# Kernel optimization log

Measured on AMD Instinct MI355X. Metric: run time of the kernel, lower is better.

The kernel has to match this reference:

```python
import jax, jax.numpy as jnp
import numpy as np
from jax import lax

B, T, N, C, AD, HW, KS, KT = 32, 8, 196, 768, 192, 14, 3, 3
EPS = 1e-5

def _groupnorm1(x, gamma, beta, axes):
    # GroupNorm(1, C): normalize over channel+spatial dims per sample
    mu = jnp.mean(x, axis=axes, keepdims=True)
    var = jnp.mean((x - mu) ** 2, axis=axes, keepdims=True)
    xn = (x - mu) * lax.rsqrt(var + EPS)
    shape = [1] * x.ndim
    shape[1] = -1
    return xn * gamma.reshape(shape) + beta.reshape(shape)

def setup_inputs() -> dict:
    key = jax.random.key(0)
    ks = jax.random.split(key, 16)
    s = 0.02
    return {
        'x': jax.random.normal(ks[0], (B, T, N + 1, C), jnp.float32),
        'w_down': jax.random.normal(ks[1], (C, AD), jnp.float32) * s,
        'b_down': jnp.zeros((AD,), jnp.float32),
        'w_sdw': jax.random.normal(ks[2], (AD, 1, KS, KS), jnp.float32) * s,
        'w_spw': jax.random.normal(ks[3], (AD, AD), jnp.float32) * s,  # [out,in]
        'g_snorm': jnp.ones((AD,), jnp.float32),
        'b_snorm': jnp.zeros((AD,), jnp.float32),
        'w_diff': jax.random.normal(ks[4], (AD, AD), jnp.float32) * s,  # [in,out]
        'w_tdw': jax.random.normal(ks[5], (AD, 1, KT), jnp.float32) * s,
        'w_tpw': jax.random.normal(ks[6], (AD, AD), jnp.float32) * s,  # [out,in]
        'g_tnorm': jnp.ones((AD,), jnp.float32),
        'b_tnorm': jnp.zeros((AD,), jnp.float32),
        'w_g1': jax.random.normal(ks[7], (AD, AD), jnp.float32) * s,
        'b_g1': jnp.zeros((AD,), jnp.float32),
        'w_g2': jax.random.normal(ks[8], (AD, AD), jnp.float32) * s,
        'b_g2': jnp.zeros((AD,), jnp.float32),
        'w_up': jax.random.normal(ks[9], (AD, C), jnp.float32) * s,  # torch zero-inits; randomized for nontrivial test
        'b_up': jnp.zeros((C,), jnp.float32),
        'w_cls': jax.random.normal(ks[10], (AD, C), jnp.float32) * s,
        'b_cls': jnp.zeros((C,), jnp.float32),
    }

def reference(x, w_down, b_down, w_sdw, w_spw, g_snorm, b_snorm, w_diff,
              w_tdw, w_tpw, g_tnorm, b_tnorm, w_g1, b_g1, w_g2, b_g2,
              w_up, b_up, w_cls, b_cls):
    gelu = lambda v: jax.nn.gelu(v, approximate=False)  # torch nn.GELU default (erf)
    cls_token = x[:, :, :1, :]
    patch = x[:, :, 1:, :]
    b, t, n, _ = patch.shape
    hw = HW
    ph = patch @ w_down + b_down  # [b,t,n,ad]
    ad = ph.shape[-1]
    # spatial path: (b t) c h w
    sp = ph.reshape(b * t, hw, hw, ad).transpose(0, 3, 1, 2)
    sp = lax.conv_general_dilated(sp, w_sdw, (1, 1), 'SAME',
                                  feature_group_count=ad,
                                  dimension_numbers=('NCHW', 'OIHW', 'NCHW'))
    sp = _groupnorm1(sp, g_snorm, b_snorm, axes=(1, 2, 3))
    sp = gelu(sp)
    sp = jnp.einsum('bchw,oc->bohw', sp, w_spw)
    spatial = sp.transpose(0, 2, 3, 1).reshape(b, t, n, ad)
    # diff gating
    diff = jnp.concatenate([jnp.zeros_like(ph[:, :1]), ph[:, 1:] - ph[:, :-1]], axis=1)
    diff = diff + diff @ w_diff
    # temporal path: (b n) c t
    tp = (ph + diff).transpose(0, 2, 3, 1).reshape(b * n, ad, t)
    tp = lax.conv_general_dilated(tp, w_tdw, (1,), 'SAME',
                                  feature_group_count=ad,
                                  dimension_numbers=('NCH', 'OIH', 'NCH'))
    tp = _groupnorm1(tp, g_tnorm, b_tnorm, axes=(1, 2))
    tp = gelu(tp)
    tp = jnp.einsum('bct,oc->bot', tp, w_tpw)
    temporal = tp.reshape(b, n, ad, t).transpose(0, 3, 1, 2)
    # gate
    gi = jnp.mean(jnp.abs(diff), axis=(1, 2))  # [b, ad]
    gate = jax.nn.sigmoid(gelu(gi @ w_g1 + b_g1) @ w_g2 + b_g2)[:, None, None, :]
    fused = gate * temporal + (1.0 - gate) * spatial
    patch_out = patch + fused @ w_up + b_up
    cls_ctx = jnp.mean(fused, axis=2, keepdims=True)
    cls_out = cls_token + cls_ctx @ w_cls + b_cls
    return jnp.concatenate([cls_out, patch_out], axis=2)
```

## Files before the change

### kernel.cpp

```cpp
#include <hip/hip_runtime.h>
#include <hip/hip_bf16.h>
#include <math.h>

typedef __attribute__((ext_vector_type(8))) short s8v;
typedef __attribute__((ext_vector_type(4))) short s4v;
typedef __attribute__((ext_vector_type(4))) float f4v;

#define GN_EPS 1e-5f

__device__ __forceinline__ float s2f(short s) {
    unsigned int u = ((unsigned int)(unsigned short)s) << 16;
    float f; __builtin_memcpy(&f, &u, 4); return f;
}
__device__ __forceinline__ short f2s(float f) {
    __hip_bfloat16 h = __float2bfloat16(f);
    short s; __builtin_memcpy(&s, &h, 2); return s;
}
__device__ __forceinline__ float gelu_f(float x) {
    return 0.5f * x * (1.0f + erff(x * 0.7071067811865476f));
}
__device__ __forceinline__ void gload16(const void* g, void* l) {
    __builtin_amdgcn_global_load_lds((const __attribute__((address_space(1))) void*)g,
                                     (__attribute__((address_space(3))) void*)l,
                                     16, 0, 0);
}

__global__ void detect_kernel(const unsigned int* g_snorm_raw, int* flag) {
    if (threadIdx.x == 0) flag[0] = (g_snorm_raw[0] == 0x3F800000u) ? 1 : 0;
}

struct ConvArgs {
    const void* src[19];
    int cum[20];
};
__global__ __launch_bounds__(256)
void convert_kernel(ConvArgs a, short* __restrict__ dst, const int* __restrict__ dflag,
                    int total) {
    const int dt = dflag[0];
    int idx = blockIdx.x * 256 + threadIdx.x;
    const int stride = gridDim.x * 256;
    for (; idx < total; idx += stride) {
        int seg = 0;
        while (idx >= a.cum[seg + 1]) seg++;
        const int off = idx - a.cum[seg];
        const float v = dt ? ((const float*)a.src[seg])[off]
                           : s2f(((const short*)a.src[seg])[off]);
        dst[idx] = f2s(v);
    }
}

__global__ __launch_bounds__(256)
void transpose_kernel(const short* __restrict__ src, short* __restrict__ dst,
                      int R, int C) {
    const int idx = blockIdx.x * 256 + threadIdx.x;
    if (idx < R * C) {
        const int r = idx / C, c = idx - r * C;
        dst[c * R + r] = src[idx];
    }
}


#define AMAP_PLAIN 0
#define AMAP_X     1
#define AMAP_DIFF  2
#define EPI_BIASH 0
#define EPI_H     1
#define EPI_DIFF  2
#define EPI_UP    3

template<int K_DIM, int N_DIM, int AMAP, int EPI>
__global__ __launch_bounds__(256)
void gemm_kernel(const void* __restrict__ Asrc, const short* __restrict__ Bmat,
                 const short* __restrict__ bias, const short* __restrict__ phH,
                 const void* __restrict__ xExt, short* __restrict__ outH,
                 void* __restrict__ outExt, float* __restrict__ giOut,
                 const int* __restrict__ dflag)
{
    const int dt = dflag[0];

    __shared__ short As[2][2048];
    __shared__ short Bs[2][2048];

    const int tid  = threadIdx.x;
    const int lane = tid & 63;
    const int wave = tid >> 6;
    const int wr = wave >> 1, wc = wave & 1;
    const int m16 = lane & 15, q = lane >> 4;
    const int rowBase = blockIdx.x * 64;
    const int colBase = blockIdx.y * 64;

    const int sr = tid >> 2;
    const int ss = tid & 3;
    const int sg = ss ^ ((sr >> 1) & 3);
    const int wOff = wave * 512;

    const int agrow = rowBase + sr;
    long aBase;
    int abt7 = 0;
    if constexpr (AMAP == AMAP_X) {
        const int bt = agrow / 196;
        aBase = (long)(agrow + bt + 1) * 768 + sg * 8;
    } else if constexpr (AMAP == AMAP_DIFF) {
        aBase = (long)agrow * K_DIM + sg * 8;
        abt7 = (agrow / 196) & 7;
    } else {
        aBase = (long)agrow * K_DIM + sg * 8;
    }
    const long bBase = (long)(colBase + sr) * K_DIM + sg * 8;

    const int ra = wr * 32 + m16;
    const int rb = wc * 32 + m16;
    const int oA0 = ra * 32 + (q ^ ((ra >> 1) & 3)) * 8;
    const int oB0 = rb * 32 + (q ^ ((rb >> 1) & 3)) * 8;
    const int oA1 = oA0 + 512;
    const int oB1 = oB0 + 512;

    f4v acc[2][2] = {};
    constexpr int NK = K_DIM / 32;

    auto stage = [&](int kk, int buf) {
        if constexpr (AMAP == AMAP_PLAIN) {
            gload16((const short*)Asrc + aBase + kk, (void*)&As[buf][wOff]);
        } else if constexpr (AMAP == AMAP_X) {
            if (dt) {
                const float* xp = (const float*)Asrc + aBase + kk;
                const float4 f0 = *(const float4*)xp;
                const float4 f1 = *(const float4*)(xp + 4);
                s8v av;
                av[0] = f2s(f0.x); av[1] = f2s(f0.y); av[2] = f2s(f0.z); av[3] = f2s(f0.w);
                av[4] = f2s(f1.x); av[5] = f2s(f1.y); av[6] = f2s(f1.z); av[7] = f2s(f1.w);
                *(s8v*)&As[buf][sr * 32 + ss * 8] = av;
            } else {
                gload16((const short*)Asrc + aBase + kk, (void*)&As[buf][wOff]);
            }
        } else {
            s8v av;
            if (abt7) {
                const short* p1 = (const short*)Asrc + aBase + kk;
                const s8v v1 = *(const s8v*)p1;
                const s8v v0 = *(const s8v*)(p1 - 37632);
                #pragma unroll
                for (int j = 0; j < 8; j++) av[j] = f2s(s2f(v1[j]) - s2f(v0[j]));
            } else {
                #pragma unroll
                for (int j = 0; j < 8; j++) av[j] = 0;
            }
            *(s8v*)&As[buf][sr * 32 + ss * 8] = av;
        }
        gload16(Bmat + bBase + kk, (void*)&Bs[buf][wOff]);
    };

    stage(0, 0);
    __syncthreads();

    int cur = 0;
    for (int t = 0; t < NK; ++t) {
        if (t + 1 < NK) stage((t + 1) * 32, cur ^ 1);

        const s8v afr0 = *(const s8v*)&As[cur][oA0];
        const s8v afr1 = *(const s8v*)&As[cur][oA1];
        const s8v bfr0 = *(const s8v*)&Bs[cur][oB0];
        const s8v bfr1 = *(const s8v*)&Bs[cur][oB1];

        acc[0][0] = __builtin_amdgcn_mfma_f32_16x16x32_bf16(bfr0, afr0, acc[0][0], 0, 0, 0);
        acc[0][1] = __builtin_amdgcn_mfma_f32_16x16x32_bf16(bfr1, afr0, acc[0][1], 0, 0, 0);
        acc[1][0] = __builtin_amdgcn_mfma_f32_16x16x32_bf16(bfr0, afr1, acc[1][0], 0, 0, 0);
        acc[1][1] = __builtin_amdgcn_mfma_f32_16x16x32_bf16(bfr1, afr1, acc[1][1], 0, 0, 0);

        __syncthreads();
        cur ^= 1;
    }

    #pragma unroll
    for (int i = 0; i < 2; i++) {
        const int grow = rowBase + wr * 32 + i * 16 + m16;
        const int gcb  = colBase + wc * 32 + q * 4;

        if constexpr (EPI == EPI_BIASH) {
            #pragma unroll
            for (int j = 0; j < 2; j++) {
                const int gc = gcb + j * 16;
                const s4v bv = *(const s4v*)&bias[gc];
                s4v o;
                #pragma unroll
                for (int r = 0; r < 4; r++) o[r] = f2s(acc[i][j][r] + s2f(bv[r]));
                *(s4v*)&outH[(long)grow * N_DIM + gc] = o;
            }
        } else if constexpr (EPI == EPI_H) {
            #pragma unroll
            for (int j = 0; j < 2; j++) {
                const int gc = gcb + j * 16;
                s4v o;
                #pragma unroll
                for (int r = 0; r < 4; r++) o[r] = f2s(acc[i][j][r]);
                *(s4v*)&outH[(long)grow * N_DIM + gc] = o;
            }
        } else if constexpr (EPI == EPI_DIFF) {
            const int t = (grow / 196) & 7;
            float ga[8];
            #pragma unroll
            for (int j = 0; j < 2; j++) {
                const int gc = gcb + j * 16;
                const long pOff = (long)grow * 192 + gc;
                const s4v p1 = *(const s4v*)&phH[pOff];
                s4v p0 = p1;
                if (t > 0) p0 = *(const s4v*)&phH[pOff - 37632];
                s4v o;
                #pragma unroll
                for (int r = 0; r < 4; r++) {
                    const float phv = s2f(p1[r]);
                    const float d = (t > 0) ? (phv - s2f(p0[r])) : 0.0f;
                    const float tpmp = acc[i][j][r] + d;
                    ga[j * 4 + r] = fabsf(tpmp);
                    o[r] = f2s(tpmp + phv);
                }
                *(s4v*)&outH[pOff] = o;
            }
            #pragma unroll
            for (int mlt = 1; mlt < 16; mlt <<= 1) {
                #pragma unroll
                for (int k = 0; k < 8; k++) ga[k] += __shfl_xor(ga[k], mlt, 64);
            }
            if (m16 == 0) {
                const int b = (rowBase + wr * 32 + i * 16) / 1568;
                #pragma unroll
                for (int k = 0; k < 8; k++) {
                    const int col = colBase + wc * 32 + (k >> 2) * 16 + q * 4 + (k & 3);
                    atomicAdd(&giOut[b * 192 + col], ga[k]);
                }
            }
        } else {
            const int bt = grow / 196;
            const long orow = (long)(grow + bt + 1) * 768;
            #pragma unroll
            for (int j = 0; j < 2; j++) {
                const int gc = gcb + j * 16;
                const s4v bv = *(const s4v*)&bias[gc];
                if (dt) {
                    const float4 xv = *(const float4*)((const float*)xExt + orow + gc);
                    float4 ov;
                    ov.x = xv.x + acc[i][j][0] + s2f(bv[0]);
                    ov.y = xv.y + acc[i][j][1] + s2f(bv[1]);
                    ov.z = xv.z + acc[i][j][2] + s2f(bv[2]);
                    ov.w = xv.w + acc[i][j][3] + s2f(bv[3]);
                    *(float4*)((float*)outExt + orow + gc) = ov;
                } else {
                    const s4v xv = *(const s4v*)((const short*)xExt + orow + gc);
                    s4v ov;
                    #pragma unroll
                    for (int r = 0; r < 4; r++)
                        ov[r] = f2s(s2f(xv[r]) + acc[i][j][r] + s2f(bv[r]));
                    *(s4v*)((short*)outExt + orow + gc) = ov;
                }
            }
        }
    }
}

__global__ __launch_bounds__(1024, 4)
void spatial_kernel(const short* __restrict__ ph, const short* __restrict__ w_sdw,
                    const short* __restrict__ g_s, const short* __restrict__ b_s,
                    short* __restrict__ snorm)
{
    __shared__ short tile[196 * 192];
    __shared__ short wkT[9 * 192];
    __shared__ float gsl[192], bsl[192];
    __shared__ float redA[16], redB[16];
    __shared__ float stats[2];

    const int bt = blockIdx.x, tid = threadIdx.x;
    const short* Pg = ph + (long)bt * 37632;

    for (int i = tid; i < 4704; i += 1024)
        *(s8v*)&tile[i * 8] = *(const s8v*)&Pg[i * 8];
    for (int i = tid; i < 1728; i += 1024) {
        const int c = i / 9, tap = i - c * 9;
        wkT[tap * 192 + c] = w_sdw[i];
    }
    if (tid < 192) { gsl[tid] = s2f(g_s[tid]); bsl[tid] = s2f(b_s[tid]); }
    __syncthreads();

    float val[5][8];
    float lsum = 0.f, lsq = 0.f;
    #pragma unroll
    for (int it = 0; it < 5; it++) {
        const int i = tid + it * 1024;
        #pragma unroll
        for (int k = 0; k < 8; k++) val[it][k] = 0.f;
        if (i < 4704) {
            const int n = i / 24, c8 = i - n * 24;
            const int h = n / 14, w = n - (n / 14) * 14;
            float a[8] = {0.f,0.f,0.f,0.f,0.f,0.f,0.f,0.f};
            #pragma unroll
            for (int tap = 0; tap < 9; tap++) {
                const int dh = tap / 3 - 1, dw = tap % 3 - 1;
                const int hh = h + dh, ww = w + dw;
                if (hh >= 0 && hh < 14 && ww >= 0 && ww < 14) {
                    s8v iv = *(const s8v*)&tile[(hh * 14 + ww) * 192 + c8 * 8];
                    s8v wv = *(const s8v*)&wkT[tap * 192 + c8 * 8];
                    #pragma unroll
                    for (int k = 0; k < 8; k++) a[k] += s2f(iv[k]) * s2f(wv[k]);
                }
            }
            #pragma unroll
            for (int k = 0; k < 8; k++) {
                val[it][k] = a[k]; lsum += a[k]; lsq += a[k] * a[k];
            }
        }
    }
    #pragma unroll
    for (int d = 1; d < 64; d <<= 1) {
        lsum += __shfl_xor(lsum, d, 64);
        lsq  += __shfl_xor(lsq,  d, 64);
    }
    if ((tid & 63) == 0) { redA[tid >> 6] = lsum; redB[tid >> 6] = lsq; }
    __syncthreads();
    if (tid < 64) {
        float s = (tid < 16) ? redA[tid] : 0.f;
        float qq = (tid < 16) ? redB[tid] : 0.f;
        #pragma unroll
        for (int d = 1; d < 16; d <<= 1) {
            s  += __shfl_xor(s,  d, 64);
            qq += __shfl_xor(qq, d, 64);
        }
        if (tid == 0) {
            const float inv = 1.0f / 37632.0f;
            const float mean = s * inv;
            const float var  = qq * inv - mean * mean;
            stats[0] = mean; stats[1] = rsqrtf(var + GN_EPS);
        }
    }
    __syncthreads();
    const float mean = stats[0], rstd = stats[1];
    short* Og = snorm + (long)bt * 37632;
    #pragma unroll
    for (int it = 0; it < 5; it++) {
        const int i = tid + it * 1024;
        if (i < 4704) {
            const int c8 = i - (i / 24) * 24;
            s8v o;
            #pragma unroll
            for (int k = 0; k < 8; k++) {
                const int c = c8 * 8 + k;
                const float y = (val[it][k] - mean) * rstd * gsl[c] + bsl[c];
                o[k] = f2s(gelu_f(y));
            }
            *(s8v*)&Og[i * 8] = o;
        }
    }
}

__global__ __launch_bounds__(192)
void temporal_kernel(const short* __restrict__ tp, const short* __restrict__ w_tdw,
                     const short* __restrict__ g_t, const short* __restrict__ b_t,
                     short* __restrict__ tnorm)
{
    const int bn = blockIdx.x;
    const int c = threadIdx.x;
    const int b = bn / 196, n = bn - (bn / 196) * 196;
    const long base = ((long)b * 8 * 196 + n) * 192 + c;
    const long ts = 196 * 192;
    float v[8], o[8];
    #pragma unroll
    for (int t = 0; t < 8; t++) v[t] = s2f(tp[base + t * ts]);
    const float w0 = s2f(w_tdw[c * 3]), w1 = s2f(w_tdw[c * 3 + 1]), w2 = s2f(w_tdw[c * 3 + 2]);
    #pragma unroll
    for (int t = 0; t < 8; t++) {
        float a = v[t] * w1;
        if (t > 0) a += v[t - 1] * w0;
        if (t < 7) a += v[t + 1] * w2;
        o[t] = a;
    }
    float lsum = 0.f, lsq = 0.f;
    #pragma unroll
    for (int t = 0; t < 8; t++) { lsum += o[t]; lsq += o[t] * o[t]; }
    __shared__ float red1[192], red2[192];
    red1[c] = lsum; red2[c] = lsq;
    __syncthreads();
    for (int s = 96; s > 2; s >>= 1) {
        if (c < s) { red1[c] += red1[c + s]; red2[c] += red2[c + s]; }
        __syncthreads();
    }
    const float mean = (red1[0] + red1[1] + red1[2]) * (1.0f / 1536.0f);
    const float var  = (red2[0] + red2[1] + red2[2]) * (1.0f / 1536.0f) - mean * mean;
    const float rstd = rsqrtf(var + GN_EPS);
    const float gg = s2f(g_t[c]), bb = s2f(b_t[c]);
    #pragma unroll
    for (int t = 0; t < 8; t++) {
        const float y = (o[t] - mean) * rstd * gg + bb;
        tnorm[base + t * ts] = f2s(gelu_f(y));
    }
}

__global__ __launch_bounds__(192)
void gate_kernel(const float* __restrict__ gi, const short* __restrict__ w_g1,
                 const short* __restrict__ b_g1, const short* __restrict__ w_g2,
                 const short* __restrict__ b_g2, float* __restrict__ gate)
{
    const int b = blockIdx.x, o = threadIdx.x;
    __shared__ float s0[192], s1[192];
    s0[o] = gi[b * 192 + o] * (1.0f / 1568.0f);
    __syncthreads();
    float a = s2f(b_g1[o]);
    for (int cc = 0; cc < 192; cc++) a += s0[cc] * s2f(w_g1[cc * 192 + o]);
    s1[o] = gelu_f(a);
    __syncthreads();
    float a2 = s2f(b_g2[o]);
    for (int cc = 0; cc < 192; cc++) a2 += s1[cc] * s2f(w_g2[cc * 192 + o]);
    gate[b * 192 + o] = 1.0f / (1.0f + expf(-a2));
}

__global__ __launch_bounds__(192)
void fuse_kernel(const short* __restrict__ temporal, const short* __restrict__ spatial,
                 const float* __restrict__ gate, short* __restrict__ fused,
                 float* __restrict__ cls_sum)
{
    const int bt = blockIdx.x;
    const int b = bt >> 3;
    const int tid = threadIdx.x;
    const int c8 = tid >> 3, sub = tid & 7;
    float g[8];
    {
        const float4* gp = (const float4*)&gate[b * 192 + c8 * 8];
        float4 ga = gp[0], gb = gp[1];
        g[0]=ga.x; g[1]=ga.y; g[2]=ga.z; g[3]=ga.w;
        g[4]=gb.x; g[5]=gb.y; g[6]=gb.z; g[7]=gb.w;
    }
    float part[8] = {0.f,0.f,0.f,0.f,0.f,0.f,0.f,0.f};
    for (int n = sub; n < 196; n += 8) {
        const long off = ((long)bt * 196 + n) * 192 + c8 * 8;
        s8v tv = *(const s8v*)(temporal + off);
        s8v sv = *(const s8v*)(spatial + off);
        s8v fv;
        #pragma unroll
        for (int k = 0; k < 8; k++) {
            const float f = g[k] * s2f(tv[k]) + (1.0f - g[k]) * s2f(sv[k]);
            fv[k] = f2s(f);
            part[k] += f;
        }
        *(s8v*)(fused + off) = fv;
    }
    #pragma unroll
    for (int d = 1; d < 8; d <<= 1) {
        #pragma unroll
        for (int k = 0; k < 8; k++) part[k] += __shfl_xor(part[k], d, 64);
    }
    if (sub == 0) {
        #pragma unroll
        for (int k = 0; k < 8; k++)
            cls_sum[bt * 192 + c8 * 8 + k] = part[k] * (1.0f / 196.0f);
    }
}

__global__ __launch_bounds__(256)
void cls_kernel(const float* __restrict__ cls_sum, const short* __restrict__ w_cls,
                const short* __restrict__ b_cls, const void* __restrict__ x,
                void* __restrict__ out, const int* __restrict__ dflag)
{
    const int dt = dflag[0];
    const int bt = blockIdx.x, tid = threadIdx.x;
    __shared__ float ctx[192];
    if (tid < 192) ctx[tid] = cls_sum[bt * 192 + tid];
    __syncthreads();
    for (int oc = tid; oc < 768; oc += 256) {
        float a = s2f(b_cls[oc]);
        for (int cc = 0; cc < 192; cc++) a += ctx[cc] * s2f(w_cls[cc * 768 + oc]);
        const long oi = (long)bt * 197 * 768 + oc;
        if (dt) ((float*)out)[oi] = ((const float*)x)[oi] + a;
        else    ((short*)out)[oi] = f2s(s2f(((const short*)x)[oi]) + a);
    }
}

extern "C" void kernel_launch(void* const* d_in, const int* in_sizes, int n_in,
                              void* d_out, int out_size, void* d_ws, size_t ws_size,
                              hipStream_t stream) {
    const void* x = d_in[0];

    const long F = 50176L * 192L;
    short* wsS = (short*)d_ws;
    short* P = wsS;
    short* Q = wsS + F;
    short* R = wsS + 2 * F;
    short* S = wsS + 3 * F;
    short* W = wsS + 4 * F;
    int cum[20]; cum[0] = 0;
    for (int i = 1; i <= 19; i++) cum[i] = cum[i - 1] + in_sizes[i];
    const int totalW = cum[19];

    short* WT   = W + ((totalW + 7) & ~7);
    short* wdT  = WT;
    short* wdfT = WT + 147456;
    short* wupT = WT + 147456 + 36864;

    float* smalls = (float*)(WT + 331776);
    float* gi      = smalls;
    float* gate    = smalls + 6144;
    float* cls_sum = smalls + 12288;
    int*   dflag   = (int*)(smalls + 61440);

    const short* b_down = W + cum[1];
    const short* w_sdw  = W + cum[2];
    const short* w_spw  = W + cum[3];
    const short* g_sn   = W + cum[4];
    const short* b_sn   = W + cum[5];
    const short* w_tdw  = W + cum[7];
    const short* w_tpw  = W + cum[8];
    const short* g_tn   = W + cum[9];
    const short* b_tn   = W + cum[10];
    const short* w_g1   = W + cum[11];
    const short* b_g1   = W + cum[12];
    const short* w_g2   = W + cum[13];
    const short* b_g2   = W + cum[14];
    const short* b_up   = W + cum[16];
    const short* w_cls  = W + cum[17];
    const short* b_cls  = W + cum[18];

    hipMemsetAsync(gi, 0, 6144 * sizeof(float), stream);
    detect_kernel<<<1, 64, 0, stream>>>((const unsigned int*)d_in[5], dflag);

    ConvArgs ca;
    for (int i = 0; i < 19; i++) ca.src[i] = d_in[i + 1];
    for (int i = 0; i < 20; i++) ca.cum[i] = cum[i];
    convert_kernel<<<618, 256, 0, stream>>>(ca, W, dflag, totalW);

    transpose_kernel<<<576, 256, 0, stream>>>(W + cum[0],  wdT,  768, 192);
    transpose_kernel<<<144, 256, 0, stream>>>(W + cum[6],  wdfT, 192, 192);
    transpose_kernel<<<576, 256, 0, stream>>>(W + cum[15], wupT, 192, 768);

    dim3 g3(784, 3), g12(784, 12);

    gemm_kernel<768, 192, AMAP_X, EPI_BIASH>
        <<<g3, 256, 0, stream>>>(x, wdT, b_down, nullptr, nullptr, P, nullptr, nullptr, dflag);
    spatial_kernel<<<256, 1024, 0, stream>>>(P, w_sdw, g_sn, b_sn, R);
    gemm_kernel<192, 192, AMAP_PLAIN, EPI_H>
        <<<g3, 256, 0, stream>>>(R, w_spw, nullptr, nullptr, nullptr, S, nullptr, nullptr, dflag);
    gemm_kernel<192, 192, AMAP_DIFF, EPI_DIFF>
        <<<g3, 256, 0, stream>>>(P, wdfT, nullptr, P, nullptr, Q, nullptr, gi, dflag);
    temporal_kernel<<<6272, 192, 0, stream>>>(Q, w_tdw, g_tn, b_tn, R);
    gemm_kernel<192, 192, AMAP_PLAIN, EPI_H>
        <<<g3, 256, 0, stream>>>(R, w_tpw, nullptr, nullptr, nullptr, Q, nullptr, nullptr, dflag);
    gate_kernel<<<32, 192, 0, stream>>>(gi, w_g1, b_g1, w_g2, b_g2, gate);
    fuse_kernel<<<256, 192, 0, stream>>>(Q, S, gate, R, cls_sum);
    gemm_kernel<192, 768, AMAP_PLAIN, EPI_UP>
        <<<g12, 256, 0, stream>>>(R, wupT, b_up, nullptr, x, nullptr, d_out, nullptr, dflag);
    cls_kernel<<<256, 256, 0, stream>>>(cls_sum, w_cls, b_cls, x, d_out, dflag);
}
```

Baseline: 620.5 us.

## Retile GEMMs to full-width blocks with triple-buffered async LDS pipeline

The GEMM kernel is templated on block tile size. The 192-wide GEMMs now use 64x192 tiles so each A tile is loaded only once, and the up-projection uses 128x128 tiles. The main loop becomes a 3-stage LDS pipeline with explicit vmcnt waits and raw barriers instead of a double buffer with __syncthreads. The fp32 A and diff paths prefetch one step ahead in registers, and the x read and output write in the epilogue use nontemporal loads and stores. Together these aim to cut redundant A reads and hide global-load latency, at the cost of more registers and LDS per block, which may lower occupancy.

```diff
diff --git a/kernel.cpp b/kernel.cpp
--- a/kernel.cpp
+++ b/kernel.cpp
@@ -24,6 +24,15 @@
                                      (__attribute__((address_space(3))) void*)l,
                                      16, 0, 0);
 }
+template<int N> __device__ __forceinline__ void wait_vm() {
+    if constexpr (N == 0) asm volatile("s_waitcnt vmcnt(0)" ::: "memory");
+    else if constexpr (N == 4) asm volatile("s_waitcnt vmcnt(4)" ::: "memory");
+    else if constexpr (N == 5) asm volatile("s_waitcnt vmcnt(5)" ::: "memory");
+    else if constexpr (N == 6) asm volatile("s_waitcnt vmcnt(6)" ::: "memory");
+    else asm volatile("s_waitcnt vmcnt(0)" ::: "memory");
+}
+__device__ __forceinline__ void wait_lgkm0() { asm volatile("s_waitcnt lgkmcnt(0)" ::: "memory"); }
+__device__ __forceinline__ void bar() { __builtin_amdgcn_s_barrier(); }
 
 __global__ void detect_kernel(const unsigned int* g_snorm_raw, int* flag) {
     if (threadIdx.x == 0) flag[0] = (g_snorm_raw[0] == 0x3F800000u) ? 1 : 0;
@@ -68,139 +77,234 @@
 #define EPI_DIFF  2
 #define EPI_UP    3
 
-template<int K_DIM, int N_DIM, int AMAP, int EPI>
-__global__ __launch_bounds__(256)
+template<int BM, int BN, int K_DIM, int N_DIM, int AMAP, int EPI>
+__global__ __launch_bounds__(256, 3)
 void gemm_kernel(const void* __restrict__ Asrc, const short* __restrict__ Bmat,
                  const short* __restrict__ bias, const short* __restrict__ phH,
                  const void* __restrict__ xExt, short* __restrict__ outH,
                  void* __restrict__ outExt, float* __restrict__ giOut,
                  const int* __restrict__ dflag)
 {
+    constexpr int WR = BM / 2, WC = BN / 2;
+    constexpr int FM = WR / 16, FN = WC / 16;
+    constexpr int AL = BM / 64;
+    constexpr int BL = BN / 64;
+    constexpr int NK = K_DIM / 32;
+    constexpr int ASZ = BM * 32, BSZ = BN * 32;
+    constexpr int GL = AL + BL;
+    constexpr int RL = 2 * AL + BL;
+
     const int dt = dflag[0];
 
-    __shared__ short As[2][2048];
-    __shared__ short Bs[2][2048];
+    __shared__ short As[3 * ASZ];
+    __shared__ short Bs[3 * BSZ];
 
     const int tid  = threadIdx.x;
     const int lane = tid & 63;
     const int wave = tid >> 6;
     const int wr = wave >> 1, wc = wave & 1;
     const int m16 = lane & 15, q = lane >> 4;
-    const int rowBase = blockIdx.x * 64;
-    const int colBase = blockIdx.y * 64;
+    const int rowBase = blockIdx.x * BM;
+    const int colBase = blockIdx.y * BN;
 
     const int sr = tid >> 2;
     const int ss = tid & 3;
     const int sg = ss ^ ((sr >> 1) & 3);
     const int wOff = wave * 512;
 
-    const int agrow = rowBase + sr;
-    long aBase;
-    int abt7 = 0;
-    if constexpr (AMAP == AMAP_X) {
-        const int bt = agrow / 196;
-        aBase = (long)(agrow + bt + 1) * 768 + sg * 8;
-    } else if constexpr (AMAP == AMAP_DIFF) {
-        aBase = (long)agrow * K_DIM + sg * 8;
-        abt7 = (agrow / 196) & 7;
+    long aBase[AL]; int abt7[AL];
+    #pragma unroll
+    for (int l = 0; l < AL; l++) {
+        const int grow = rowBase + sr + 64 * l;
+        if constexpr (AMAP == AMAP_X) {
+            const int bt = grow / 196;
+            aBase[l] = (long)(grow + bt + 1) * 768 + sg * 8;
+            abt7[l] = 0;
+        } else if constexpr (AMAP == AMAP_DIFF) {
+            aBase[l] = (long)grow * K_DIM + sg * 8;
+            abt7[l] = (grow / 196) & 7;
+        } else {
+            aBase[l] = (long)grow * K_DIM + sg * 8;
+            abt7[l] = 0;
+        }
+    }
+    long bBase[BL];
+    #pragma unroll
+    for (int l = 0; l < BL; l++)
+        bBase[l] = (long)(colBase + sr + 64 * l) * K_DIM + sg * 8;
+
+    const int ra0 = wr * WR + m16;
+    const int rb0 = wc * WC + m16;
+    const int oA0 = ra0 * 32 + (q ^ ((ra0 >> 1) & 3)) * 8;
+    const int oB0 = rb0 * 32 + (q ^ ((rb0 >> 1) & 3)) * 8;
+
+    f4v acc[FM][FN] = {};
+
+    auto compute = [&](int aOff, int bOff) {
+        s8v af[FM], bf[FN];
+        #pragma unroll
+        for (int i = 0; i < FM; i++) af[i] = *(const s8v*)&As[aOff + oA0 + i * 512];
+        #pragma unroll
+        for (int j = 0; j < FN; j++) bf[j] = *(const s8v*)&Bs[bOff + oB0 + j * 512];
+        #pragma unroll
+        for (int i = 0; i < FM; i++)
+            #pragma unroll
+            for (int j = 0; j < FN; j++)
+                acc[i][j] = __builtin_amdgcn_mfma_f32_16x16x32_bf16(bf[j], af[i], acc[i][j], 0, 0, 0);
+    };
+    auto gstageB = [&](int kk, int buf) {
+        #pragma unroll
+        for (int l = 0; l < BL; l++)
+            gload16(Bmat + bBase[l] + kk, (void*)&Bs[buf * BSZ + l * 2048 + wOff]);
+    };
+    auto gstageA = [&](int kk, int buf) {
+        #pragma unroll
+        for (int l = 0; l < AL; l++)
+            gload16((const short*)Asrc + aBase[l] + kk, (void*)&As[buf * ASZ + l * 2048 + wOff]);
+    };
+
+    if constexpr (AMAP == AMAP_PLAIN) {
+        gstageA(0, 0);  gstageB(0, 0);
+        gstageA(32, 1); gstageB(32, 1);
+        wait_vm<GL>(); bar();
+        int bi = 0;
+        for (int t = 0; t < NK - 2; ++t) {
+            int b2 = bi + 2; if (b2 >= 3) b2 -= 3;
+            gstageA((t + 2) * 32, b2); gstageB((t + 2) * 32, b2);
+            compute(bi * ASZ, bi * BSZ);
+            wait_vm<GL>(); bar();
+            bi = (bi + 1 == 3) ? 0 : bi + 1;
+        }
+        compute(bi * ASZ, bi * BSZ);
+        wait_vm<0>(); bar();
+        bi = (bi + 1 == 3) ? 0 : bi + 1;
+        compute(bi * ASZ, bi * BSZ);
+    } else if constexpr (AMAP == AMAP_X) {
+        if (dt == 0) {
+            gstageA(0, 0);  gstageB(0, 0);
+            gstageA(32, 1); gstageB(32, 1);
+            wait_vm<GL>(); bar();
+            int bi = 0;
+            for (int t = 0; t < NK - 2; ++t) {
+                int b2 = bi + 2; if (b2 >= 3) b2 -= 3;
+                gstageA((t + 2) * 32, b2); gstageB((t + 2) * 32, b2);
+                compute(bi * ASZ, bi * BSZ);
+                wait_vm<GL>(); bar();
+                bi = (bi + 1 == 3) ? 0 : bi + 1;
+            }
+            compute(bi * ASZ, bi * BSZ);
+            wait_vm<0>(); bar();
+            bi = (bi + 1 == 3) ? 0 : bi + 1;
+            compute(bi * ASZ, bi * BSZ);
+        } else {
+            f4v ra0v, ra1v, rb0v, rb1v;
+            auto loadA = [&](int kk, f4v& r0, f4v& r1) {
+                const float* xp = (const float*)Asrc + aBase[0] + kk;
+                r0 = __builtin_nontemporal_load((const f4v*)xp);
+                r1 = __builtin_nontemporal_load((const f4v*)(xp + 4));
+            };
+            auto writeA = [&](int idx, const f4v& r0, const f4v& r1) {
+                s8v av;
+                av[0] = f2s(r0.x); av[1] = f2s(r0.y); av[2] = f2s(r0.z); av[3] = f2s(r0.w);
+                av[4] = f2s(r1.x); av[5] = f2s(r1.y); av[6] = f2s(r1.z); av[7] = f2s(r1.w);
+                *(s8v*)&As[idx * ASZ + tid * 8] = av;
+            };
+            loadA(0, ra0v, ra1v); gstageB(0, 0);
+            wait_vm<0>();
+            writeA(0, ra0v, ra1v);
+            loadA(32, ra0v, ra1v); gstageB(32, 1);
+            wait_lgkm0(); bar();
+            int bi = 0;
+            for (int t = 0; t < NK - 2; ++t) {
+                int b2 = bi + 2; if (b2 >= 3) b2 -= 3;
+                loadA((t + 2) * 32, rb0v, rb1v); gstageB((t + 2) * 32, b2);
+                compute((t & 1) * ASZ, bi * BSZ);
+                wait_vm<RL>();
+                writeA((t + 1) & 1, ra0v, ra1v);
+                wait_lgkm0(); bar();
+                ra0v = rb0v; ra1v = rb1v;
+                bi = (bi + 1 == 3) ? 0 : bi + 1;
+            }
+            compute(((NK - 2) & 1) * ASZ, bi * BSZ);
+            wait_vm<0>();
+            writeA((NK - 1) & 1, ra0v, ra1v);
+            wait_lgkm0(); bar();
+            bi = (bi + 1 == 3) ? 0 : bi + 1;
+            compute(((NK - 1) & 1) * ASZ, bi * BSZ);
+        }
     } else {
-        aBase = (long)agrow * K_DIM + sg * 8;
-    }
-    const long bBase = (long)(colBase + sr) * K_DIM + sg * 8;
-
-    const int ra = wr * 32 + m16;
-    const int rb = wc * 32 + m16;
-    const int oA0 = ra * 32 + (q ^ ((ra >> 1) & 3)) * 8;
-    const int oB0 = rb * 32 + (q ^ ((rb >> 1) & 3)) * 8;
-    const int oA1 = oA0 + 512;
-    const int oB1 = oB0 + 512;
-
-    f4v acc[2][2] = {};
-    constexpr int NK = K_DIM / 32;
-
-    auto stage = [&](int kk, int buf) {
-        if constexpr (AMAP == AMAP_PLAIN) {
-            gload16((const short*)Asrc + aBase + kk, (void*)&As[buf][wOff]);
-        } else if constexpr (AMAP == AMAP_X) {
-            if (dt) {
-                const float* xp = (const float*)Asrc + aBase + kk;
-                const float4 f0 = *(const float4*)xp;
-                const float4 f1 = *(const float4*)(xp + 4);
-                s8v av;
-                av[0] = f2s(f0.x); av[1] = f2s(f0.y); av[2] = f2s(f0.z); av[3] = f2s(f0.w);
-                av[4] = f2s(f1.x); av[5] = f2s(f1.y); av[6] = f2s(f1.z); av[7] = f2s(f1.w);
-                *(s8v*)&As[buf][sr * 32 + ss * 8] = av;
-            } else {
-                gload16((const short*)Asrc + aBase + kk, (void*)&As[buf][wOff]);
-            }
-        } else {
+        s8v ra1v, ra0v, rb1v, rb0v;
+        auto loadA = [&](int kk, s8v& v1, s8v& v0) {
+            const short* p1 = (const short*)Asrc + aBase[0] + kk;
+            const short* p0 = p1 - (abt7[0] ? 37632 : 0);
+            v1 = *(const s8v*)p1;
+            v0 = *(const s8v*)p0;
+        };
+        auto writeA = [&](int idx, const s8v& v1, const s8v& v0) {
             s8v av;
-            if (abt7) {
-                const short* p1 = (const short*)Asrc + aBase + kk;
-                const s8v v1 = *(const s8v*)p1;
-                const s8v v0 = *(const s8v*)(p1 - 37632);
+            if (abt7[0]) {
                 #pragma unroll
                 for (int j = 0; j < 8; j++) av[j] = f2s(s2f(v1[j]) - s2f(v0[j]));
             } else {
                 #pragma unroll
                 for (int j = 0; j < 8; j++) av[j] = 0;
             }
-            *(s8v*)&As[buf][sr * 32 + ss * 8] = av;
-        }
-        gload16(Bmat + bBase + kk, (void*)&Bs[buf][wOff]);
-    };
-
-    stage(0, 0);
-    __syncthreads();
-
-    int cur = 0;
-    for (int t = 0; t < NK; ++t) {
-        if (t + 1 < NK) stage((t + 1) * 32, cur ^ 1);
-
-        const s8v afr0 = *(const s8v*)&As[cur][oA0];
-        const s8v afr1 = *(const s8v*)&As[cur][oA1];
-        const s8v bfr0 = *(const s8v*)&Bs[cur][oB0];
-        const s8v bfr1 = *(const s8v*)&Bs[cur][oB1];
-
-        acc[0][0] = __builtin_amdgcn_mfma_f32_16x16x32_bf16(bfr0, afr0, acc[0][0], 0, 0, 0);
-        acc[0][1] = __builtin_amdgcn_mfma_f32_16x16x32_bf16(bfr1, afr0, acc[0][1], 0, 0, 0);
-        acc[1][0] = __builtin_amdgcn_mfma_f32_16x16x32_bf16(bfr0, afr1, acc[1][0], 0, 0, 0);
-        acc[1][1] = __builtin_amdgcn_mfma_f32_16x16x32_bf16(bfr1, afr1, acc[1][1], 0, 0, 0);
-
-        __syncthreads();
-        cur ^= 1;
-    }
-
-    #pragma unroll
-    for (int i = 0; i < 2; i++) {
-        const int grow = rowBase + wr * 32 + i * 16 + m16;
-        const int gcb  = colBase + wc * 32 + q * 4;
+            *(s8v*)&As[idx * ASZ + tid * 8] = av;
+        };
+        loadA(0, ra1v, ra0v); gstageB(0, 0);
+        wait_vm<0>();
+        writeA(0, ra1v, ra0v);
+        loadA(32, ra1v, ra0v); gstageB(32, 1);
+        wait_lgkm0(); bar();
+        int bi = 0;
+        for (int t = 0; t < NK - 2; ++t) {
+            int b2 = bi + 2; if (b2 >= 3) b2 -= 3;
+            loadA((t + 2) * 32, rb1v, rb0v); gstageB((t + 2) * 32, b2);
+            compute((t & 1) * ASZ, bi * BSZ);
+            wait_vm<RL>();
+            writeA((t + 1) & 1, ra1v, ra0v);
+            wait_lgkm0(); bar();
+            ra1v = rb1v; ra0v = rb0v;
+            bi = (bi + 1 == 3) ? 0 : bi + 1;
+        }
+        compute(((NK - 2) & 1) * ASZ, bi * BSZ);
+        wait_vm<0>();
+        writeA((NK - 1) & 1, ra1v, ra0v);
+        wait_lgkm0(); bar();
+        bi = (bi + 1 == 3) ? 0 : bi + 1;
+        compute(((NK - 1) & 1) * ASZ, bi * BSZ);
+    }
+
+    #pragma unroll
+    for (int fi = 0; fi < FM; fi++) {
+        const int grow = rowBase + wr * WR + fi * 16 + m16;
+        const int gcb  = colBase + wc * WC + q * 4;
 
         if constexpr (EPI == EPI_BIASH) {
             #pragma unroll
-            for (int j = 0; j < 2; j++) {
-                const int gc = gcb + j * 16;
+            for (int fj = 0; fj < FN; fj++) {
+                const int gc = gcb + fj * 16;
                 const s4v bv = *(const s4v*)&bias[gc];
                 s4v o;
                 #pragma unroll
-                for (int r = 0; r < 4; r++) o[r] = f2s(acc[i][j][r] + s2f(bv[r]));
+                for (int r = 0; r < 4; r++) o[r] = f2s(acc[fi][fj][r] + s2f(bv[r]));
                 *(s4v*)&outH[(long)grow * N_DIM + gc] = o;
             }
         } else if constexpr (EPI == EPI_H) {
             #pragma unroll
-            for (int j = 0; j < 2; j++) {
-                const int gc = gcb + j * 16;
+            for (int fj = 0; fj < FN; fj++) {
+                const int gc = gcb + fj * 16;
                 s4v o;
                 #pragma unroll
-                for (int r = 0; r < 4; r++) o[r] = f2s(acc[i][j][r]);
+                for (int r = 0; r < 4; r++) o[r] = f2s(acc[fi][fj][r]);
                 *(s4v*)&outH[(long)grow * N_DIM + gc] = o;
             }
         } else if constexpr (EPI == EPI_DIFF) {
             const int t = (grow / 196) & 7;
-            float ga[8];
-            #pragma unroll
-            for (int j = 0; j < 2; j++) {
-                const int gc = gcb + j * 16;
+            float ga[FN * 4];
+            #pragma unroll
+            for (int fj = 0; fj < FN; fj++) {
+                const int gc = gcb + fj * 16;
                 const long pOff = (long)grow * 192 + gc;
                 const s4v p1 = *(const s4v*)&phH[pOff];
                 s4v p0 = p1;
@@ -210,8 +314,8 @@
                 for (int r = 0; r < 4; r++) {
                     const float phv = s2f(p1[r]);
                     const float d = (t > 0) ? (phv - s2f(p0[r])) : 0.0f;
-                    const float tpmp = acc[i][j][r] + d;
-                    ga[j * 4 + r] = fabsf(tpmp);
+                    const float tpmp = acc[fi][fj][r] + d;
+                    ga[fj * 4 + r] = fabsf(tpmp);
                     o[r] = f2s(tpmp + phv);
                 }
                 *(s4v*)&outH[pOff] = o;
@@ -219,13 +323,13 @@
             #pragma unroll
             for (int mlt = 1; mlt < 16; mlt <<= 1) {
                 #pragma unroll
-                for (int k = 0; k < 8; k++) ga[k] += __shfl_xor(ga[k], mlt, 64);
+                for (int k = 0; k < FN * 4; k++) ga[k] += __shfl_xor(ga[k], mlt, 64);
             }
             if (m16 == 0) {
-                const int b = (rowBase + wr * 32 + i * 16) / 1568;
+                const int b = (rowBase + wr * WR + fi * 16) / 1568;
                 #pragma unroll
-                for (int k = 0; k < 8; k++) {
-                    const int col = colBase + wc * 32 + (k >> 2) * 16 + q * 4 + (k & 3);
+                for (int k = 0; k < FN * 4; k++) {
+                    const int col = colBase + wc * WC + (k >> 2) * 16 + q * 4 + (k & 3);
                     atomicAdd(&giOut[b * 192 + col], ga[k]);
                 }
             }
@@ -233,23 +337,24 @@
             const int bt = grow / 196;
             const long orow = (long)(grow + bt + 1) * 768;
             #pragma unroll
-            for (int j = 0; j < 2; j++) {
-                const int gc = gcb + j * 16;
+            for (int fj = 0; fj < FN; fj++) {
+                const int gc = gcb + fj * 16;
                 const s4v bv = *(const s4v*)&bias[gc];
                 if (dt) {
-                    const float4 xv = *(const float4*)((const float*)xExt + orow + gc);
-                    float4 ov;
-                    ov.x = xv.x + acc[i][j][0] + s2f(bv[0]);
-                    ov.y = xv.y + acc[i][j][1] + s2f(bv[1]);
-                    ov.z = xv.z + acc[i][j][2] + s2f(bv[2]);
-                    ov.w = xv.w + acc[i][j][3] + s2f(bv[3]);
-                    *(float4*)((float*)outExt + orow + gc) = ov;
+                    const f4v xv = __builtin_nontemporal_load(
+                        (const f4v*)((const float*)xExt + orow + gc));
+                    f4v ov;
+                    ov.x = xv.x + acc[fi][fj][0] + s2f(bv[0]);
+                    ov.y = xv.y + acc[fi][fj][1] + s2f(bv[1]);
+                    ov.z = xv.z + acc[fi][fj][2] + s2f(bv[2]);
+                    ov.w = xv.w + acc[fi][fj][3] + s2f(bv[3]);
+                    __builtin_nontemporal_store(ov, (f4v*)((float*)outExt + orow + gc));
                 } else {
                     const s4v xv = *(const s4v*)((const short*)xExt + orow + gc);
                     s4v ov;
                     #pragma unroll
                     for (int r = 0; r < 4; r++)
-                        ov[r] = f2s(s2f(xv[r]) + acc[i][j][r] + s2f(bv[r]));
+                        ov[r] = f2s(s2f(xv[r]) + acc[fi][fj][r] + s2f(bv[r]));
                     *(s4v*)((short*)outExt + orow + gc) = ov;
                 }
             }
@@ -421,8 +526,8 @@
     const int c8 = tid >> 3, sub = tid & 7;
     float g[8];
     {
-        const float4* gp = (const float4*)&gate[b * 192 + c8 * 8];
-        float4 ga = gp[0], gb = gp[1];
+        const f4v* gp = (const f4v*)&gate[b * 192 + c8 * 8];
+        f4v ga = gp[0], gb = gp[1];
         g[0]=ga.x; g[1]=ga.y; g[2]=ga.z; g[3]=ga.w;
         g[4]=gb.x; g[5]=gb.y; g[6]=gb.z; g[7]=gb.w;
     }
@@ -527,21 +632,19 @@
     transpose_kernel<<<144, 256, 0, stream>>>(W + cum[6],  wdfT, 192, 192);
     transpose_kernel<<<576, 256, 0, stream>>>(W + cum[15], wupT, 192, 768);
 
-    dim3 g3(784, 3), g12(784, 12);
-
-    gemm_kernel<768, 192, AMAP_X, EPI_BIASH>
-        <<<g3, 256, 0, stream>>>(x, wdT, b_down, nullptr, nullptr, P, nullptr, nullptr, dflag);
+    gemm_kernel<64, 192, 768, 192, AMAP_X, EPI_BIASH>
+        <<<dim3(784, 1), 256, 0, stream>>>(x, wdT, b_down, nullptr, nullptr, P, nullptr, nullptr, dflag);
     spatial_kernel<<<256, 1024, 0, stream>>>(P, w_sdw, g_sn, b_sn, R);
-    gemm_kernel<192, 192, AMAP_PLAIN, EPI_H>
-        <<<g3, 256, 0, stream>>>(R, w_spw, nullptr, nullptr, nullptr, S, nullptr, nullptr, dflag);
-    gemm_kernel<192, 192, AMAP_DIFF, EPI_DIFF>
-        <<<g3, 256, 0, stream>>>(P, wdfT, nullptr, P, nullptr, Q, nullptr, gi, dflag);
+    gemm_kernel<64, 192, 192, 192, AMAP_PLAIN, EPI_H>
+        <<<dim3(784, 1), 256, 0, stream>>>(R, w_spw, nullptr, nullptr, nullptr, S, nullptr, nullptr, dflag);
+    gemm_kernel<64, 192, 192, 192, AMAP_DIFF, EPI_DIFF>
+        <<<dim3(784, 1), 256, 0, stream>>>(P, wdfT, nullptr, P, nullptr, Q, nullptr, gi, dflag);
     temporal_kernel<<<6272, 192, 0, stream>>>(Q, w_tdw, g_tn, b_tn, R);
-    gemm_kernel<192, 192, AMAP_PLAIN, EPI_H>
-        <<<g3, 256, 0, stream>>>(R, w_tpw, nullptr, nullptr, nullptr, Q, nullptr, nullptr, dflag);
+    gemm_kernel<64, 192, 192, 192, AMAP_PLAIN, EPI_H>
+        <<<dim3(784, 1), 256, 0, stream>>>(R, w_tpw, nullptr, nullptr, nullptr, Q, nullptr, nullptr, dflag);
     gate_kernel<<<32, 192, 0, stream>>>(gi, w_g1, b_g1, w_g2, b_g2, gate);
     fuse_kernel<<<256, 192, 0, stream>>>(Q, S, gate, R, cls_sum);
-    gemm_kernel<192, 768, AMAP_PLAIN, EPI_UP>
-        <<<g12, 256, 0, stream>>>(R, wupT, b_up, nullptr, x, nullptr, d_out, nullptr, dflag);
+    gemm_kernel<128, 128, 192, 768, AMAP_PLAIN, EPI_UP>
+        <<<dim3(392, 6), 256, 0, stream>>>(R, wupT, b_up, nullptr, x, nullptr, d_out, nullptr, dflag);
     cls_kernel<<<256, 256, 0, stream>>>(cls_sum, w_cls, b_cls, x, d_out, dflag);
 }
```

Result: no change. 615.7 us (-0.8%).
